# Optimization experiments

Measured on AMD Instinct MI355X. Metric: run time of the kernel, lower is better.

The kernel has to match this reference:

```python
import jax, jax.numpy as jnp
import numpy as np

EPS = 1e-5  # torch BatchNorm1d default eps

def _bn(y, gamma, beta):
    # training-mode BatchNorm1d over batch axis (biased variance), per timestep
    mu = jnp.mean(y, axis=0, keepdims=True)
    var = jnp.mean((y - mu) ** 2, axis=0, keepdims=True)
    return gamma * (y - mu) * jax.lax.rsqrt(var + EPS) + beta

def setup_inputs() -> dict:
    key = jax.random.key(0)
    ks = jax.random.split(key, 16)
    T, B, I, H = 512, 64, 512, 512
    s = 1.0 / np.sqrt(H)
    def w(k, shape):
        return jax.random.uniform(k, shape, jnp.float32, -s, s)
    return {
        "x": jax.random.normal(ks[0], (T, B, I), jnp.float32),
        "h0": jnp.zeros((1, B, H), jnp.float32),
        "W_z_w": w(ks[1], (H, H)), "W_z_b": w(ks[2], (H,)),
        "U_z_w": w(ks[3], (H, I)), "U_z_b": w(ks[4], (H,)),
        "W_r_w": w(ks[5], (H, H)), "W_r_b": w(ks[6], (H,)),
        "U_r_w": w(ks[7], (H, I)), "U_r_b": w(ks[8], (H,)),
        "W_h_w": w(ks[9], (H, H)), "W_h_b": w(ks[10], (H,)),
        "U_h_w": w(ks[11], (H, I)), "U_h_b": w(ks[12], (H,)),
        "bn_gamma": jnp.ones((H,), jnp.float32),
        "bn_beta": jnp.zeros((H,), jnp.float32),
    }

def reference(x, h0, W_z_w, W_z_b, U_z_w, U_z_b, W_r_w, W_r_b, U_r_w, U_r_b,
              W_h_w, W_h_b, U_h_w, U_h_b, bn_gamma, bn_beta):
    T, B, _ = x.shape
    H = h0.shape[-1]
    # precompute input projections for all timesteps (parallelizable part)
    uz = jnp.einsum('tbi,hi->tbh', x, U_z_w) + U_z_b  # [T,B,H]
    ur = jnp.einsum('tbi,hi->tbh', x, U_r_w) + U_r_b
    uh = jnp.einsum('tbi,hi->tbh', x, U_h_w) + U_h_b

    def step(h, inp):
        uz_t, ur_t, uh_t = inp
        z = jax.nn.sigmoid(h @ W_z_w.T + W_z_b + _bn(uz_t, bn_gamma, bn_beta))
        r = jax.nn.sigmoid(h @ W_r_w.T + W_r_b + _bn(ur_t, bn_gamma, bn_beta))
        new_state = jnp.tanh((r * h) @ W_h_w.T + W_h_b + _bn(uh_t, bn_gamma, bn_beta))
        h_new = (1.0 - z) * h + z * new_state
        return h_new, h_new

    _, hs = jax.lax.scan(step, h0[0], (uz, ur, uh))  # hs: [T,B,H]
    output = hs.reshape(T, B, 1, H)   # [T, B, directions=1, H]
    h_out = hs.reshape(1, T, B, H)    # faithful to torch code's final `h`
    return output, h_out
```

## Files before the change

kernel.cpp:

```cpp
#include <hip/hip_runtime.h>
#include <hip/hip_bf16.h>


using bf16x8 = __attribute__((ext_vector_type(8))) short;
using f32x4  = __attribute__((ext_vector_type(4))) float;
using fvec4  = __attribute__((ext_vector_type(4))) float;
using s16x4  = __attribute__((ext_vector_type(4))) short;

#define NWG 32

static __device__ __forceinline__ unsigned short f2bf(float f) {
  union { float ff; unsigned int i; } v; v.ff = f;
  unsigned int x = v.i;
  x += 0x7fffu + ((x >> 16) & 1u);
  return (unsigned short)(x >> 16);
}
static __device__ __forceinline__ float h2f(unsigned short u) {
  union { unsigned short s; _Float16 h; } v; v.s = u; return (float)v.h;
}
static __device__ __forceinline__ unsigned short f2h(float f) {
  union { unsigned short s; _Float16 h; } v; v.h = (_Float16)f; return v.s;
}
static __device__ __forceinline__ float sigmoidf_(float x) {
  return 1.0f / (1.0f + __expf(-x));
}
static __device__ __forceinline__ float tanhf_(float x) {
  return 2.0f / (1.0f + __expf(-2.0f * x)) - 1.0f;
}

__global__ __launch_bounds__(256) void proj_gemm(
    const float* __restrict__ x,
    const float* __restrict__ Uz, const float* __restrict__ Ur,
    const float* __restrict__ Uh,
    const float* __restrict__ Wzb, const float* __restrict__ Wrb,
    const float* __restrict__ Whb,
    const float* __restrict__ gamma, const float* __restrict__ beta,
    unsigned short* __restrict__ ubz, unsigned short* __restrict__ ubr,
    unsigned short* __restrict__ ubh)
{
  const int mt = blockIdx.x, nt = blockIdx.y, mat = blockIdx.z;
  const float* U  = (mat == 0) ? Uz  : (mat == 1 ? Ur  : Uh);
  const float* Wb = (mat == 0) ? Wzb : (mat == 1 ? Wrb : Whb);
  unsigned short* uo = (mat == 0) ? ubz : (mat == 1 ? ubr : ubh);

  __shared__ short lA[4096];
  __shared__ short lB[4096];

  const int tid = threadIdx.x;
  const int wave = tid >> 6, lane = tid & 63;
  const int fl = lane & 15, kseg = lane >> 4;

  f32x4 acc[4];
  #pragma unroll
  for (int n = 0; n < 4; ++n) acc[n] = f32x4{0.f, 0.f, 0.f, 0.f};

  const float* xb = x + (size_t)mt * 64 * 512;
  const float* Ub = U + (size_t)nt * 64 * 512;

  for (int kt = 0; kt < 8; ++kt) {
    __syncthreads();
    #pragma unroll
    for (int c = 0; c < 2; ++c) {
      const int chunk = tid + 256 * c;
      const int row = chunk >> 3, kc = chunk & 7;
      const int lb = row * 128 + ((kc * 16) ^ ((row & 7) << 4));
      {
        const float* g = xb + (size_t)row * 512 + kt * 64 + kc * 8;
        fvec4 a0 = *(const fvec4*)g, a1 = *(const fvec4*)(g + 4);
        bf16x8 p;
        p[0] = (short)f2bf(a0[0]); p[1] = (short)f2bf(a0[1]);
        p[2] = (short)f2bf(a0[2]); p[3] = (short)f2bf(a0[3]);
        p[4] = (short)f2bf(a1[0]); p[5] = (short)f2bf(a1[1]);
        p[6] = (short)f2bf(a1[2]); p[7] = (short)f2bf(a1[3]);
        *(bf16x8*)((char*)lA + lb) = p;
      }
      {
        const float* g = Ub + (size_t)row * 512 + kt * 64 + kc * 8;
        fvec4 a0 = *(const fvec4*)g, a1 = *(const fvec4*)(g + 4);
        bf16x8 p;
        p[0] = (short)f2bf(a0[0]); p[1] = (short)f2bf(a0[1]);
        p[2] = (short)f2bf(a0[2]); p[3] = (short)f2bf(a0[3]);
        p[4] = (short)f2bf(a1[0]); p[5] = (short)f2bf(a1[1]);
        p[6] = (short)f2bf(a1[2]); p[7] = (short)f2bf(a1[3]);
        *(bf16x8*)((char*)lB + lb) = p;
      }
    }
    __syncthreads();
    #pragma unroll
    for (int kk = 0; kk < 2; ++kk) {
      const int ar = wave * 16 + fl;
      bf16x8 af = *(const bf16x8*)((char*)lA + ar * 128 +
                    ((kk * 64 + kseg * 16) ^ ((ar & 7) << 4)));
      #pragma unroll
      for (int n = 0; n < 4; ++n) {
        const int br = n * 16 + fl;
        bf16x8 bfr = *(const bf16x8*)((char*)lB + br * 128 +
                      ((kk * 64 + kseg * 16) ^ ((br & 7) << 4)));
        acc[n] = __builtin_amdgcn_mfma_f32_16x16x32_bf16(af, bfr, acc[n], 0, 0, 0);
      }
    }
  }

  float sn[4], qn[4];
  #pragma unroll
  for (int n = 0; n < 4; ++n) {
    sn[n] = acc[n][0] + acc[n][1] + acc[n][2] + acc[n][3];
    qn[n] = acc[n][0]*acc[n][0] + acc[n][1]*acc[n][1]
          + acc[n][2]*acc[n][2] + acc[n][3]*acc[n][3];
    sn[n] += __shfl_xor(sn[n], 16); qn[n] += __shfl_xor(qn[n], 16);
    sn[n] += __shfl_xor(sn[n], 32); qn[n] += __shfl_xor(qn[n], 32);
  }
  __syncthreads();
  float* sArr = (float*)lA;
  float* qArr = (float*)lB;
  if (kseg == 0) {
    #pragma unroll
    for (int n = 0; n < 4; ++n) {
      sArr[wave * 64 + n * 16 + fl] = sn[n];
      qArr[wave * 64 + n * 16 + fl] = qn[n];
    }
  }
  __syncthreads();

  const int c0 = nt * 64;
  const int b0 = wave * 16 + kseg * 4;
  #pragma unroll
  for (int n = 0; n < 4; ++n) {
    const int idx = n * 16 + fl;
    const float s = sArr[idx] + sArr[64+idx] + sArr[128+idx] + sArr[192+idx];
    const float q = qArr[idx] + qArr[64+idx] + qArr[128+idx] + qArr[192+idx];
    const float mu = s * 0.015625f;
    const float rs = rsqrtf(q * 0.015625f - mu * mu + 1e-5f);
    const int col = c0 + idx;
    const float gb  = gamma[col] * rs;
    const float ofs = beta[col] + Wb[col] - gb * mu;
    s16x4 pk;
    #pragma unroll
    for (int i = 0; i < 4; ++i)
      pk[i] = (short)f2h(gb * acc[n][i] + ofs);
    *(s16x4*)(uo + ((size_t)mt * 512 + col) * 64 + b0) = pk;
  }
}

__global__ __launch_bounds__(256) void gru_scan(
    const float* __restrict__ h0,
    const float* __restrict__ Wz, const float* __restrict__ Wr,
    const float* __restrict__ Wh,
    const unsigned short* __restrict__ ubz, const unsigned short* __restrict__ ubr,
    const unsigned short* __restrict__ ubh,
    unsigned int* __restrict__ hbuf, unsigned int* __restrict__ rhbuf,
    unsigned int* __restrict__ flags, float* __restrict__ out)
{
  const int wg = blockIdx.x;
  const int tid = threadIdx.x;
  const int wave = tid >> 6, lane = tid & 63;
  const int fl = lane & 15, kseg = lane >> 4;
  const int col = wg * 16 + fl;
  const int row0 = wave * 16 + kseg * 4;
  const int hrow = wave * 16 + fl;

  __shared__ short lW[24576];

  for (int c = tid; c < 3072; c += 256) {
    const int m = c >> 10, rem = c & 1023;
    const int r = rem >> 6, kc = rem & 63;
    const float* W = (m == 0) ? Wz : (m == 1 ? Wr : Wh);
    const float* g = W + (size_t)(wg * 16 + r) * 512 + kc * 8;
    bf16x8 p;
    #pragma unroll
    for (int j = 0; j < 8; ++j) p[j] = (short)f2bf(g[j]);
    *(bf16x8*)((char*)lW + m * 16384 + r * 1024 + ((kc * 16) ^ ((r & 7) << 4))) = p;
  }

  auto publish4 = [&](unsigned int* buf, const float v0, const float v1,
                      const float v2, const float v3) {
    float vv[4] = {v0, v1, v2, v3};
    #pragma unroll
    for (int i = 0; i < 4; ++i) {
      unsigned int mine = f2bf(vv[i]);
      unsigned int other = (unsigned int)__shfl_xor((int)mine, 1);
      unsigned int word = (fl & 1) ? ((mine << 16) | other)
                                   : (mine | (other << 16));
      if ((fl & 1) == (i & 1))
        __hip_atomic_store(&buf[(row0 + i) * 256 + (col >> 1)], word,
                           __ATOMIC_RELAXED, __HIP_MEMORY_SCOPE_AGENT);
    }
  };
  auto read_frag = [&](const unsigned int* buf, int kk) -> bf16x8 {
    const unsigned long long* p =
        (const unsigned long long*)buf + hrow * 128 + kk * 8 + kseg * 2;
    union { unsigned long long q[2]; bf16x8 f; } u;
    u.q[0] = __hip_atomic_load(p,     __ATOMIC_RELAXED, __HIP_MEMORY_SCOPE_AGENT);
    u.q[1] = __hip_atomic_load(p + 1, __ATOMIC_RELAXED, __HIP_MEMORY_SCOPE_AGENT);
    return u.f;
  };
  auto wait_ev = [&](unsigned int ev) {
    if (lane < NWG) {
      while (__hip_atomic_load(&flags[lane << 5], __ATOMIC_RELAXED,
                               __HIP_MEMORY_SCOPE_AGENT) < ev) {}
    }
    asm volatile("" ::: "memory");
  };
  auto arrive = [&](unsigned int ev) {
    asm volatile("s_waitcnt vmcnt(0)" ::: "memory");
    __syncthreads();
    if (tid == 0)
      __hip_atomic_store(&flags[wg << 5], ev, __ATOMIC_RELAXED,
                         __HIP_MEMORY_SCOPE_AGENT);
  };

  float hown[4];
  #pragma unroll
  for (int i = 0; i < 4; ++i)
    hown[i] = h0[(size_t)(row0 + i) * 512 + col];
  publish4(hbuf, hown[0], hown[1], hown[2], hown[3]);
  arrive(1u);

  float uzv[4], urv[4], uhv[4];
  {
    const size_t ub = ((size_t)col) * 64 + row0;
    s16x4 az = *(const s16x4*)(ubz + ub);
    s16x4 ar = *(const s16x4*)(ubr + ub);
    s16x4 ah = *(const s16x4*)(ubh + ub);
    #pragma unroll
    for (int i = 0; i < 4; ++i) {
      uzv[i] = h2f((unsigned short)az[i]);
      urv[i] = h2f((unsigned short)ar[i]);
      uhv[i] = h2f((unsigned short)ah[i]);
    }
  }

  for (int t = 0; t < 512; ++t) {
    wait_ev(2 * t + 1);

    bf16x8 af[16];
    #pragma unroll
    for (int kk = 0; kk < 16; ++kk)
      af[kk] = read_frag(hbuf, kk);

    f32x4 zacc = f32x4{0.f,0.f,0.f,0.f}, racc = f32x4{0.f,0.f,0.f,0.f};
    #pragma unroll
    for (int kk = 0; kk < 16; ++kk) {
      const int wof = (kk * 64 + kseg * 16) ^ ((fl & 7) << 4);
      bf16x8 b0 = *(const bf16x8*)((const char*)lW + fl * 1024 + wof);
      bf16x8 b1 = *(const bf16x8*)((const char*)lW + 16384 + fl * 1024 + wof);
      zacc = __builtin_amdgcn_mfma_f32_16x16x32_bf16(af[kk], b0, zacc, 0, 0, 0);
      racc = __builtin_amdgcn_mfma_f32_16x16x32_bf16(af[kk], b1, racc, 0, 0, 0);
    }

    float z4[4], r4[4];
    #pragma unroll
    for (int i = 0; i < 4; ++i) {
      z4[i] = sigmoidf_(zacc[i] + uzv[i]);
      r4[i] = sigmoidf_(racc[i] + urv[i]);
    }

    publish4(rhbuf, r4[0] * hown[0], r4[1] * hown[1],
                    r4[2] * hown[2], r4[3] * hown[3]);

    arrive(2u * t + 2u);
    wait_ev(2 * t + 2);

    #pragma unroll
    for (int kk = 0; kk < 16; ++kk)
      af[kk] = read_frag(rhbuf, kk);

    f32x4 hacc = f32x4{0.f,0.f,0.f,0.f};
    #pragma unroll
    for (int kk = 0; kk < 16; ++kk) {
      const int wof = (kk * 64 + kseg * 16) ^ ((fl & 7) << 4);
      bf16x8 b2 = *(const bf16x8*)((const char*)lW + 32768 + fl * 1024 + wof);
      hacc = __builtin_amdgcn_mfma_f32_16x16x32_bf16(af[kk], b2, hacc, 0, 0, 0);
    }

    float hn[4];
    #pragma unroll
    for (int i = 0; i < 4; ++i) {
      const float nb = tanhf_(hacc[i] + uhv[i]);
      hn[i] = (1.f - z4[i]) * hown[i] + z4[i] * nb;
      hown[i] = hn[i];
    }
    publish4(hbuf, hn[0], hn[1], hn[2], hn[3]);

    arrive(2u * t + 3u);

    if (t + 1 < 512) {
      const size_t ub = ((size_t)(t + 1) * 512 + col) * 64 + row0;
      s16x4 az = *(const s16x4*)(ubz + ub);
      s16x4 ar = *(const s16x4*)(ubr + ub);
      s16x4 ah = *(const s16x4*)(ubh + ub);
      #pragma unroll
      for (int i = 0; i < 4; ++i) {
        uzv[i] = h2f((unsigned short)az[i]);
        urv[i] = h2f((unsigned short)ar[i]);
        uhv[i] = h2f((unsigned short)ah[i]);
      }
    }
    {
      const size_t tb = (size_t)t * 64 * 512;
      #pragma unroll
      for (int i = 0; i < 4; ++i) {
        const size_t o = tb + (size_t)(row0 + i) * 512 + col;
        const float v = hn[i];
        out[o] = v;
        out[16777216 + o] = v;
      }
    }
  }
}

extern "C" void kernel_launch(void* const* d_in, const int* in_sizes, int n_in,
                              void* d_out, int out_size, void* d_ws, size_t ws_size,
                              hipStream_t stream) {
  (void)in_sizes; (void)n_in; (void)out_size; (void)ws_size;
  const float* x   = (const float*)d_in[0];
  const float* h0  = (const float*)d_in[1];
  const float* Wz  = (const float*)d_in[2];
  const float* Wzb = (const float*)d_in[3];
  const float* Uz  = (const float*)d_in[4];
  const float* Wr  = (const float*)d_in[6];
  const float* Wrb = (const float*)d_in[7];
  const float* Ur  = (const float*)d_in[8];
  const float* Wh  = (const float*)d_in[10];
  const float* Whb = (const float*)d_in[11];
  const float* Uh  = (const float*)d_in[12];
  const float* gam = (const float*)d_in[14];
  const float* bet = (const float*)d_in[15];
  float* out = (float*)d_out;

  char* ws = (char*)d_ws;
  unsigned int*   flags = (unsigned int*)(ws);
  unsigned int*   hbuf  = (unsigned int*)(ws + 8192);
  unsigned int*   rhbuf = (unsigned int*)(ws + 8192 + 65536);
  unsigned short* uzb   = (unsigned short*)(ws + 262144);
  unsigned short* urb   = (unsigned short*)(ws + 262144 + 33554432);
  unsigned short* uhb   = (unsigned short*)(ws + 262144 + 2ll * 33554432);

  hipMemsetAsync(flags, 0, 8192, stream);

  dim3 gp(512, 8, 3);
  proj_gemm<<<gp, 256, 0, stream>>>(x, Uz, Ur, Uh, Wzb, Wrb, Whb,
                                    gam, bet, uzb, urb, uhb);
  gru_scan<<<dim3(NWG), 256, 0, stream>>>(h0, Wz, Wr, Wh, uzb, urb, uhb,
                                          hbuf, rhbuf, flags, out);
}
```

Before: 5.885 ms.

## Replace flag barriers with epoch-tagged data words and publish r*h earlier

```diff
diff --git a/kernel.cpp b/kernel.cpp
--- a/kernel.cpp
+++ b/kernel.cpp
@@ -148,8 +148,9 @@
     const float* __restrict__ Wh,
     const unsigned short* __restrict__ ubz, const unsigned short* __restrict__ ubr,
     const unsigned short* __restrict__ ubh,
-    unsigned int* __restrict__ hbuf, unsigned int* __restrict__ rhbuf,
-    unsigned int* __restrict__ flags, float* __restrict__ out)
+    unsigned long long* __restrict__ hbuf,
+    unsigned long long* __restrict__ rhbuf,
+    float* __restrict__ out)
 {
   const int wg = blockIdx.x;
   const int tid = threadIdx.x;
@@ -171,9 +172,10 @@
     for (int j = 0; j < 8; ++j) p[j] = (short)f2bf(g[j]);
     *(bf16x8*)((char*)lW + m * 16384 + r * 1024 + ((kc * 16) ^ ((r & 7) << 4))) = p;
   }
-
-  auto publish4 = [&](unsigned int* buf, const float v0, const float v1,
-                      const float v2, const float v3) {
+  __syncthreads();
+
+  auto publish4 = [&](unsigned long long* buf, unsigned int ev, const float v0,
+                      const float v1, const float v2, const float v3) {
     float vv[4] = {v0, v1, v2, v3};
     #pragma unroll
     for (int i = 0; i < 4; ++i) {
@@ -182,39 +184,45 @@
       unsigned int word = (fl & 1) ? ((mine << 16) | other)
                                    : (mine | (other << 16));
       if ((fl & 1) == (i & 1))
-        __hip_atomic_store(&buf[(row0 + i) * 256 + (col >> 1)], word,
+        __hip_atomic_store(&buf[(row0 + i) * 256 + (col >> 1)],
+                           ((unsigned long long)ev << 32) | (unsigned long long)word,
                            __ATOMIC_RELAXED, __HIP_MEMORY_SCOPE_AGENT);
     }
   };
-  auto read_frag = [&](const unsigned int* buf, int kk) -> bf16x8 {
-    const unsigned long long* p =
-        (const unsigned long long*)buf + hrow * 128 + kk * 8 + kseg * 2;
-    union { unsigned long long q[2]; bf16x8 f; } u;
-    u.q[0] = __hip_atomic_load(p,     __ATOMIC_RELAXED, __HIP_MEMORY_SCOPE_AGENT);
-    u.q[1] = __hip_atomic_load(p + 1, __ATOMIC_RELAXED, __HIP_MEMORY_SCOPE_AGENT);
-    return u.f;
-  };
-  auto wait_ev = [&](unsigned int ev) {
-    if (lane < NWG) {
-      while (__hip_atomic_load(&flags[lane << 5], __ATOMIC_RELAXED,
-                               __HIP_MEMORY_SCOPE_AGENT) < ev) {}
-    }
-    asm volatile("" ::: "memory");
-  };
-  auto arrive = [&](unsigned int ev) {
-    asm volatile("s_waitcnt vmcnt(0)" ::: "memory");
-    __syncthreads();
-    if (tid == 0)
-      __hip_atomic_store(&flags[wg << 5], ev, __ATOMIC_RELAXED,
-                         __HIP_MEMORY_SCOPE_AGENT);
+
+  auto poll8 = [&](const unsigned long long* buf, unsigned int ev, int kk0,
+                   bf16x8* dst) {
+    const unsigned long long* base = buf + hrow * 256 + kseg * 4;
+    unsigned long long w[32];
+    for (;;) {
+      #pragma unroll
+      for (int j = 0; j < 8; ++j) {
+        #pragma unroll
+        for (int q = 0; q < 4; ++q)
+          w[j * 4 + q] = __hip_atomic_load(base + (kk0 + j) * 16 + q,
+                                           __ATOMIC_RELAXED,
+                                           __HIP_MEMORY_SCOPE_AGENT);
+      }
+      bool ok = true;
+      #pragma unroll
+      for (int j = 0; j < 32; ++j)
+        ok &= ((unsigned int)(w[j] >> 32) == ev);
+      if (ok) break;
+    }
+    #pragma unroll
+    for (int j = 0; j < 8; ++j) {
+      union { unsigned int d[4]; bf16x8 f; } u;
+      #pragma unroll
+      for (int q = 0; q < 4; ++q) u.d[q] = (unsigned int)w[j * 4 + q];
+      dst[j] = u.f;
+    }
   };
 
   float hown[4];
   #pragma unroll
   for (int i = 0; i < 4; ++i)
     hown[i] = h0[(size_t)(row0 + i) * 512 + col];
-  publish4(hbuf, hown[0], hown[1], hown[2], hown[3]);
-  arrive(1u);
+  publish4(hbuf, 1u, hown[0], hown[1], hown[2], hown[3]);
 
   float uzv[4], urv[4], uhv[4];
   {
@@ -231,39 +239,38 @@
   }
 
   for (int t = 0; t < 512; ++t) {
-    wait_ev(2 * t + 1);
+    const unsigned int ev = (unsigned int)t + 1u;
 
     bf16x8 af[16];
-    #pragma unroll
-    for (int kk = 0; kk < 16; ++kk)
-      af[kk] = read_frag(hbuf, kk);
-
-    f32x4 zacc = f32x4{0.f,0.f,0.f,0.f}, racc = f32x4{0.f,0.f,0.f,0.f};
+    poll8(hbuf, ev, 0, af);
+    poll8(hbuf, ev, 8, af + 8);
+
+    f32x4 racc = f32x4{0.f,0.f,0.f,0.f};
+    #pragma unroll
+    for (int kk = 0; kk < 16; ++kk) {
+      const int wof = (kk * 64 + kseg * 16) ^ ((fl & 7) << 4);
+      bf16x8 b1 = *(const bf16x8*)((const char*)lW + 16384 + fl * 1024 + wof);
+      racc = __builtin_amdgcn_mfma_f32_16x16x32_bf16(af[kk], b1, racc, 0, 0, 0);
+    }
+    float r4[4];
+    #pragma unroll
+    for (int i = 0; i < 4; ++i) r4[i] = sigmoidf_(racc[i] + urv[i]);
+    publish4(rhbuf, ev, r4[0] * hown[0], r4[1] * hown[1],
+                        r4[2] * hown[2], r4[3] * hown[3]);
+
+    f32x4 zacc = f32x4{0.f,0.f,0.f,0.f};
     #pragma unroll
     for (int kk = 0; kk < 16; ++kk) {
       const int wof = (kk * 64 + kseg * 16) ^ ((fl & 7) << 4);
       bf16x8 b0 = *(const bf16x8*)((const char*)lW + fl * 1024 + wof);
-      bf16x8 b1 = *(const bf16x8*)((const char*)lW + 16384 + fl * 1024 + wof);
       zacc = __builtin_amdgcn_mfma_f32_16x16x32_bf16(af[kk], b0, zacc, 0, 0, 0);
-      racc = __builtin_amdgcn_mfma_f32_16x16x32_bf16(af[kk], b1, racc, 0, 0, 0);
-    }
-
-    float z4[4], r4[4];
-    #pragma unroll
-    for (int i = 0; i < 4; ++i) {
-      z4[i] = sigmoidf_(zacc[i] + uzv[i]);
-      r4[i] = sigmoidf_(racc[i] + urv[i]);
-    }
-
-    publish4(rhbuf, r4[0] * hown[0], r4[1] * hown[1],
-                    r4[2] * hown[2], r4[3] * hown[3]);
-
-    arrive(2u * t + 2u);
-    wait_ev(2 * t + 2);
-
-    #pragma unroll
-    for (int kk = 0; kk < 16; ++kk)
-      af[kk] = read_frag(rhbuf, kk);
+    }
+    float z4[4];
+    #pragma unroll
+    for (int i = 0; i < 4; ++i) z4[i] = sigmoidf_(zacc[i] + uzv[i]);
+
+    poll8(rhbuf, ev, 0, af);
+    poll8(rhbuf, ev, 8, af + 8);
 
     f32x4 hacc = f32x4{0.f,0.f,0.f,0.f};
     #pragma unroll
@@ -280,9 +287,7 @@
       hn[i] = (1.f - z4[i]) * hown[i] + z4[i] * nb;
       hown[i] = hn[i];
     }
-    publish4(hbuf, hn[0], hn[1], hn[2], hn[3]);
-
-    arrive(2u * t + 3u);
+    publish4(hbuf, ev + 1u, hn[0], hn[1], hn[2], hn[3]);
 
     if (t + 1 < 512) {
       const size_t ub = ((size_t)(t + 1) * 512 + col) * 64 + row0;
@@ -329,18 +334,15 @@
   float* out = (float*)d_out;
 
   char* ws = (char*)d_ws;
-  unsigned int*   flags = (unsigned int*)(ws);
-  unsigned int*   hbuf  = (unsigned int*)(ws + 8192);
-  unsigned int*   rhbuf = (unsigned int*)(ws + 8192 + 65536);
-  unsigned short* uzb   = (unsigned short*)(ws + 262144);
-  unsigned short* urb   = (unsigned short*)(ws + 262144 + 33554432);
-  unsigned short* uhb   = (unsigned short*)(ws + 262144 + 2ll * 33554432);
-
-  hipMemsetAsync(flags, 0, 8192, stream);
+  unsigned long long* hbuf  = (unsigned long long*)(ws);
+  unsigned long long* rhbuf = (unsigned long long*)(ws + 131072);
+  unsigned short*     uzb   = (unsigned short*)(ws + 262144);
+  unsigned short*     urb   = (unsigned short*)(ws + 262144 + 33554432);
+  unsigned short*     uhb   = (unsigned short*)(ws + 262144 + 2ll * 33554432);
 
   dim3 gp(512, 8, 3);
   proj_gemm<<<gp, 256, 0, stream>>>(x, Uz, Ur, Uh, Wzb, Wrb, Whb,
                                     gam, bet, uzb, urb, uhb);
   gru_scan<<<dim3(NWG), 256, 0, stream>>>(h0, Wz, Wr, Wh, uzb, urb, uhb,
-                                          hbuf, rhbuf, flags, out);
-}
+                                          hbuf, rhbuf, out);
+}
```

After: 10.02 ms. 70.2% more time.
